# Kernel optimization log

Measured on AMD Instinct MI355X. Metric: run time of the kernel, lower is better.

The kernel has to match this reference:

```python
import jax, jax.numpy as jnp
import numpy as np
from jax.scipy.special import erf

B, S, D = 8, 512, 512
H = 8            # num_heads per half
DH = D // 2      # 256, per-branch model dim
DFF = 2048
HOUT = 2


def _layernorm(x, g, b, eps=1e-6):
    mu = jnp.mean(x, axis=-1, keepdims=True)
    var = jnp.mean(jnp.square(x - mu), axis=-1, keepdims=True)
    return (x - mu) / jnp.sqrt(var + eps) * g + b


def _rescale_dist(w):
    one = jnp.float32(1.0)
    return (one + jnp.exp(one)) / (one + jnp.exp(one - w))


def _mha(xin, wq, bq, wk, bk, wv, bv, wo, bo, maskf, adjoin, dist):
    b, s, dm = xin.shape
    dep = dm // H
    def heads(t):
        return t.reshape(b, s, H, dep).transpose(0, 2, 1, 3)  # (b,h,s,dep)
    q = heads(xin @ wq + bq)
    k = heads(xin @ wk + bk)
    v = heads(xin @ wv + bv)
    scores = jnp.einsum('bhqd,bhkd->bhqk', q, k)
    scale = jnp.sqrt(jnp.float32(dep))
    if dist is not None:
        scores = jax.nn.relu(scores) * _rescale_dist(dist) / scale
    else:
        scores = scores / scale
    scores = scores + maskf * jnp.float32(-1e9)
    if adjoin is not None:
        scores = scores + adjoin
    attn = jax.nn.softmax(scores, axis=-1)
    out = jnp.einsum('bhqk,bhkd->bhqd', attn, v).transpose(0, 2, 1, 3).reshape(b, s, dm)
    return out @ wo + bo, attn


def setup_inputs() -> dict:
    key = jax.random.key(0)
    ks = jax.random.split(key, 32)
    init = lambda k, shp: (jax.random.normal(k, shp, dtype=jnp.float32) * 0.02)
    inp = {
        'x': jax.random.normal(ks[0], (B, S, D), dtype=jnp.float32),
        'adjoin_matrix': jax.random.normal(ks[1], (B, 1, S, S), dtype=jnp.float32),
        'dist_matrix': jax.random.uniform(ks[2], (B, 1, S, S), dtype=jnp.float32),
        # mha1 (adjoin branch)
        'wq1': init(ks[3], (DH, DH)), 'bq1': jnp.zeros((DH,), jnp.float32),
        'wk1': init(ks[4], (DH, DH)), 'bk1': jnp.zeros((DH,), jnp.float32),
        'wv1': init(ks[5], (DH, DH)), 'bv1': jnp.zeros((DH,), jnp.float32),
        'wo1': init(ks[6], (DH, DH)), 'bo1': jnp.zeros((DH,), jnp.float32),
        # mha2 (distance branch)
        'wq2': init(ks[7], (DH, DH)), 'bq2': jnp.zeros((DH,), jnp.float32),
        'wk2': init(ks[8], (DH, DH)), 'bk2': jnp.zeros((DH,), jnp.float32),
        'wv2': init(ks[9], (DH, DH)), 'bv2': jnp.zeros((DH,), jnp.float32),
        'wo2': init(ks[10], (DH, DH)), 'bo2': jnp.zeros((DH,), jnp.float32),
        # BANLayer
        'vnet_w': init(ks[11], (DH, 2 * DH)), 'vnet_b': jnp.zeros((2 * DH,), jnp.float32),
        'qnet_w': init(ks[12], (DH, 2 * DH)), 'qnet_b': jnp.zeros((2 * DH,), jnp.float32),
        'h_mat': init(ks[13], (1, HOUT, 1, 2 * DH)),
        'h_bias': init(ks[14], (1, HOUT, 1, 1)),
        'bn_gamma': jnp.ones((D,), jnp.float32), 'bn_beta': jnp.zeros((D,), jnp.float32),
        'bn_mean': jnp.zeros((D,), jnp.float32), 'bn_var': jnp.ones((D,), jnp.float32),
        # LayerNorms
        'ln1_g': jnp.ones((D,), jnp.float32), 'ln1_b': jnp.zeros((D,), jnp.float32),
        'ln2_g': jnp.ones((D,), jnp.float32), 'ln2_b': jnp.zeros((D,), jnp.float32),
        # FFN
        'ffn_w1': init(ks[15], (D, DFF)), 'ffn_b1': jnp.zeros((DFF,), jnp.float32),
        'ffn_w2': init(ks[16], (DFF, D)), 'ffn_b2': jnp.zeros((D,), jnp.float32),
        # padding mask (int -> cast), 1 = masked
        'encoder_padding_mask': jax.random.randint(ks[17], (B, 1, 1, S), 0, 2, dtype=jnp.int32),
    }
    return inp


def reference(x, adjoin_matrix, dist_matrix,
              wq1, bq1, wk1, bk1, wv1, bv1, wo1, bo1,
              wq2, bq2, wk2, bk2, wv2, bv2, wo2, bo2,
              vnet_w, vnet_b, qnet_w, qnet_b, h_mat, h_bias,
              bn_gamma, bn_beta, bn_mean, bn_var,
              ln1_g, ln1_b, ln2_g, ln2_b,
              ffn_w1, ffn_b1, ffn_w2, ffn_b2,
              encoder_padding_mask):
    maskf = encoder_padding_mask.astype(jnp.float32)
    x1, x2 = jnp.split(x, 2, axis=-1)
    # local branch: adjoin bias, no distance
    x_l, aw_local = _mha(x1, wq1, bq1, wk1, bk1, wv1, bv1, wo1, bo1, maskf, adjoin_matrix, None)
    # global branch: relu + distance rescale, no adjoin
    x_g, aw_global = _mha(x2, wq2, bq2, wk2, bk2, wv2, bv2, wo2, bo2, maskf, None, dist_matrix)
    # BANLayer (h_out=2 <= c, eval mode; p_net is identity for rows=1)
    v_ = jax.nn.relu(x_l @ vnet_w + vnet_b)   # (B,S,2*DH)
    q_ = jax.nn.relu(x_g @ qnet_w + qnet_b)
    att_maps = jnp.einsum('xhyk,bvk,bqk->bhvq', h_mat, v_, q_) + h_bias  # (B,HOUT,S,S)
    logits = jnp.einsum('bvk,bhvq,bqk->bvk', v_, att_maps, q_)           # sum over h
    logits = (logits - bn_mean) / jnp.sqrt(bn_var + 1e-3) * bn_gamma + bn_beta
    attn_output = logits * jnp.concatenate([x_l, x_g], axis=-1)
    out1 = _layernorm(x + attn_output, ln1_g, ln1_b)
    h = out1 @ ffn_w1 + ffn_b1
    h = 0.5 * h * (1.0 + erf(h / jnp.sqrt(jnp.float32(2.0))))  # exact gelu
    ffn_out = h @ ffn_w2 + ffn_b2
    out2 = _layernorm(out1 + ffn_out, ln2_g, ln2_b)
    return (out2, aw_local, aw_global)
```

## Files before the change

### kernel.cpp

```cpp
#include <hip/hip_runtime.h>
#include <hip/hip_bf16.h>

typedef __hip_bfloat16 bf16;
typedef __attribute__((ext_vector_type(8))) short bf16x8;
typedef __attribute__((ext_vector_type(4))) float f32x4;
typedef __attribute__((ext_vector_type(4))) _Float16 f16x4;
typedef unsigned int u32;

#define BB 8
#define SS 512
#define DD 512
#define NH 8
#define DHm 256
#define DFF 2048

__device__ __forceinline__ void gl_lds16(const void* g, void* l) {
  __builtin_amdgcn_global_load_lds((const __attribute__((address_space(1))) void*)g,
                                   (__attribute__((address_space(3))) void*)l, 16, 0, 0);
}

__device__ __forceinline__ bf16x8 cvt8(const float* p) {
  union { bf16x8 v; bf16 h[8]; } u;
  float4 f0 = *(const float4*)p, f1 = *(const float4*)(p + 4);
  u.h[0]=__float2bfloat16(f0.x); u.h[1]=__float2bfloat16(f0.y);
  u.h[2]=__float2bfloat16(f0.z); u.h[3]=__float2bfloat16(f0.w);
  u.h[4]=__float2bfloat16(f1.x); u.h[5]=__float2bfloat16(f1.y);
  u.h[6]=__float2bfloat16(f1.z); u.h[7]=__float2bfloat16(f1.w);
  return u.v;
}

template<int BM, int BN, int SMODE, int BIASM, int ACT, int VTM>
__global__ __launch_bounds__(256)
void gemm2(const bf16* __restrict__ A, const bf16* __restrict__ B,
           const float* __restrict__ bias, float* __restrict__ Cf,
           bf16* __restrict__ Cb, int K, int lda, int ldb, int ldc,
           long long sA, long long sB, long long sC, int sBias,
           bf16* __restrict__ Cb2, const float* __restrict__ cscale)
{
  __shared__ bf16 As[BM * 32];
  __shared__ bf16 Bs[BN * 32];
  const int t = threadIdx.x, lane = t & 63, wave = t >> 6;
  const int l15 = lane & 15, quad = lane >> 4;
  constexpr int WMT = BM / 32, WNT = BN / 32;
  const int wm = (wave & 1) * (BM / 2), wn = (wave >> 1) * (BN / 2);
  const int row0 = blockIdx.y * BM, col0 = blockIdx.x * BN;
  const bf16* Ab = A + (long long)blockIdx.z * sA + (long long)row0 * lda;
  const bf16* Bb = B + (long long)blockIdx.z * sB + (long long)col0 * ldb;
  const int srow = wave * 16 + (lane >> 2), skc = (lane & 3) << 3;

  f32x4 acc[WMT][WNT] = {};

  for (int k0 = 0; k0 < K; k0 += 32) {
#pragma unroll
    for (int j = 0; j < BM / 64; j++)
      gl_lds16(Ab + (long long)(srow + j * 64) * lda + k0 + skc,
               (char*)As + wave * 1024 + j * 4096);
#pragma unroll
    for (int j = 0; j < BN / 64; j++)
      gl_lds16(Bb + (long long)(srow + j * 64) * ldb + k0 + skc,
               (char*)Bs + wave * 1024 + j * 4096);
    __syncthreads();
    bf16x8 af[WMT], bfr[WNT];
#pragma unroll
    for (int i = 0; i < WMT; i++) af[i]  = *(const bf16x8*)&As[(wm + i * 16 + l15) * 32 + quad * 8];
#pragma unroll
    for (int j = 0; j < WNT; j++) bfr[j] = *(const bf16x8*)&Bs[(wn + j * 16 + l15) * 32 + quad * 8];
#pragma unroll
    for (int i = 0; i < WMT; i++)
#pragma unroll
      for (int j = 0; j < WNT; j++)
        acc[i][j] = __builtin_amdgcn_mfma_f32_16x16x32_bf16(af[i], bfr[j], acc[i][j], 0, 0, 0);
    __syncthreads();
  }

  float sb = 0.f;
  if (BIASM == 2) sb = bias[0] + bias[1];
#pragma unroll
  for (int i = 0; i < WMT; i++)
#pragma unroll
    for (int j = 0; j < WNT; j++) {
      int col = col0 + wn + j * 16 + l15;
      float bv = (BIASM == 1) ? bias[(long long)blockIdx.z * sBias + col] : sb;
      float vv[4];
#pragma unroll
      for (int r = 0; r < 4; r++) {
        float v = acc[i][j][r] + bv;
        if (ACT == 1) v = fmaxf(v, 0.f);
        if (ACT == 2) v = 0.5f * v * (1.f + erff(v * 0.70710678118654752f));
        vv[r] = v;
      }
      const int rowb = row0 + wm + i * 16 + (quad << 2);
      if (VTM == 1) {
        const int bidx = rowb >> 9, kpos = rowb & 511;
        const long long zz8 = (long long)blockIdx.z * 8 + bidx;
        if (col < 512) {
          const int part = col >> 8, hh = (col >> 5) & 7, dep = col & 31;
          bf16* dst = Cb2 + (((zz8 * 8 + hh) * 2 + part) * 512 + (long long)kpos) * 32 + dep;
#pragma unroll
          for (int r = 0; r < 4; r++) dst[r * 32] = __float2bfloat16(vv[r]);
        } else {
          const int hh = (col - 512) >> 5, dep = (col - 512) & 31;
          long long vo = ((zz8 * 8 + hh) * 64 + (kpos >> 3)) * 32 + dep;
          bf16 h0 = __float2bfloat16(vv[0]), h1 = __float2bfloat16(vv[1]);
          bf16 h2 = __float2bfloat16(vv[2]), h3 = __float2bfloat16(vv[3]);
          short4 pk;
          pk.x = *(short*)&h0; pk.y = *(short*)&h1; pk.z = *(short*)&h2; pk.w = *(short*)&h3;
          *(short4*)(Cb + vo * 8 + (kpos & 7)) = pk;
        }
      } else {
#pragma unroll
        for (int r = 0; r < 4; r++) {
          long long ci = (long long)blockIdx.z * sC + (long long)(rowb + r) * ldc + col;
          if (SMODE & 1) Cf[ci] = vv[r];
          if (SMODE & 2) Cb[ci] = __float2bfloat16(vv[r]);
          if (VTM == 2) Cb2[ci] = __float2bfloat16(vv[r] * cscale[col]);
        }
      }
    }
}

__global__ __launch_bounds__(256)
void eprep(const float* __restrict__ adjoin, const float* __restrict__ dist,
           const int* __restrict__ mask, _Float16* __restrict__ EP)
{
  const int qt = blockIdx.x, kt = blockIdx.y, zz = blockIdx.z;
  const int b = zz & 7, branch = zz >> 3;
  const float* E = (branch ? dist : adjoin) + ((long long)b * SS + qt * 64) * SS + kt * 128;
  __shared__ float tile[64][129];
  const int t = threadIdx.x;
  const int r0 = t >> 5, c4 = (t & 31) * 4;
#pragma unroll
  for (int jj = 0; jj < 8; jj++) {
    int row = r0 + jj * 8;
    float4 f = *(const float4*)(E + (long long)row * SS + c4);
    tile[row][c4 + 0] = f.x; tile[row][c4 + 1] = f.y;
    tile[row][c4 + 2] = f.z; tile[row][c4 + 3] = f.w;
  }
  __syncthreads();
  const int lane = t & 63, wq = t >> 6, l15 = lane & 15, quad = lane >> 4;
  const float scale_inv = 0.17677669529663688f;
  f16x4* out = (f16x4*)EP;
#pragma unroll
  for (int kcl = 0; kcl < 8; kcl++) {
    int kk = kcl * 16 + l15;
    f16x4 o;
    if (branch == 0) {
      float mv = (float)mask[b * SS + kt * 128 + kk] * -1e9f;
#pragma unroll
      for (int r = 0; r < 4; r++)
        o[r] = (_Float16)(tile[wq * 16 + quad * 4 + r][kk] + mv);
    } else {
#pragma unroll
      for (int r = 0; r < 4; r++) {
        float ev = tile[wq * 16 + quad * 4 + r][kk];
        o[r] = (_Float16)(3.7182818284590452f / (1.f + __expf(1.f - ev)) * scale_inv);
      }
    }
    out[((((long long)zz * 8 + qt) * 4 + wq) * 32 + (kt * 8 + kcl)) * 64 + lane] = o;
  }
}

__global__ __launch_bounds__(256, 2)
void attn_fused(const bf16* __restrict__ QKF, const bf16* __restrict__ VT,
                const int* __restrict__ mask, const _Float16* __restrict__ EP,
                float* __restrict__ awl, float* __restrict__ awg,
                bf16* __restrict__ ctx1, bf16* __restrict__ ctx2)
{
  const int qt = blockIdx.x, h = blockIdx.y, zz = blockIdx.z;
  const int b = zz & 7, branch = zz >> 3;
  float* __restrict__ aw = branch ? awg : awl;
  bf16* __restrict__ ctx = branch ? ctx2 : ctx1;

  const int t = threadIdx.x, lane = t & 63, wave = t >> 6;
  const int l15 = lane & 15, quad = lane >> 4;
  __shared__ bf16x8 Vt[64][32];
  alignas(16) __shared__ bf16 Pl[4][2048];
  __shared__ float mvalf[512];

  const bf16* VTs = VT + ((long long)zz * 8 + h) * 16384;
#pragma unroll
  for (int j = 0; j < 8; j++)
    gl_lds16(VTs + (long long)t * 8 + j * 2048, (char*)Vt + wave * 1024 + j * 4096);

  { int2 m2 = *(const int2*)(mask + b * SS + t * 2);
    mvalf[t * 2]     = (float)m2.x * -1e9f;
    mvalf[t * 2 + 1] = (float)m2.y * -1e9f; }

  const int q0 = qt * 64 + wave * 16;
  const bf16* Qbase = QKF + ((long long)zz * 8 + h) * 2 * 16384;
  const bf16* Kbase = Qbase + 16384;
  bf16x8 qfrag = *(const bf16x8*)(Qbase + (long long)(q0 + l15) * 32 + quad * 8);
  __syncthreads();

  const float scale_inv = 0.17677669529663688f;
  const f16x4* Ep = (const f16x4*)EP + (((long long)zz * 8 + qt) * 4 + wave) * 2048;

  u32 eh[64];
  float rsum[4] = {0.f, 0.f, 0.f, 0.f};
  f32x4 oacc[2] = {};
  short* Pw = (short*)Pl[wave];
  const int rkey = ((l15 >> 2) ^ l15) & 3;

#pragma unroll
  for (int c = 0; c < 4; c++) {
#pragma unroll
    for (int kcl = 0; kcl < 8; kcl++) {
      const int kc = c * 8 + kcl;
      const int kpos = kc * 16 + l15;
      bf16x8 kfrag = *(const bf16x8*)(Kbase + (long long)kpos * 32 + quad * 8);
      f16x4 e4 = Ep[kc * 64 + lane];
      f32x4 a = __builtin_amdgcn_mfma_f32_16x16x32_bf16(qfrag, kfrag, f32x4{0.f,0.f,0.f,0.f}, 0, 0, 0);
      float mv = (branch == 0) ? 0.f : mvalf[kpos];
      u32 p01 = 0, p23 = 0;
#pragma unroll
      for (int r = 0; r < 4; r++) {
        float s = (branch == 0) ? fmaf(a[r], scale_inv, (float)e4[r])
                                : fmaf(fmaxf(a[r], 0.f), (float)e4[r], mv);
        float e = __expf(s);
        rsum[r] += e;
        u32 xb = __float_as_uint(e);
        u32 b16 = (xb + 0x7FFFu + ((xb >> 16) & 1u)) >> 16;
        if (r == 0)      p01 = b16;
        else if (r == 1) p01 |= b16 << 16;
        else if (r == 2) p23 = b16;
        else             p23 |= b16 << 16;
        const int key = (quad ^ r) & 3;
        const int off = (quad * 4 + r) * 256 + (((kcl * 16 + l15) * 2) ^ (key << 5));
        *(short*)((char*)Pw + off) = (short)b16;
      }
      eh[kc * 2]     = p01;
      eh[kc * 2 + 1] = p23;
    }
    __builtin_amdgcn_s_setprio(1);
#pragma unroll
    for (int k2 = 0; k2 < 4; k2++) {
      const int off = l15 * 256 + ((k2 * 64 + quad * 16) ^ (rkey << 5));
      bf16x8 afr = *(const bf16x8*)((const char*)Pw + off);
      const int blk = (c * 4 + k2) * 4 + quad;
      oacc[0] = __builtin_amdgcn_mfma_f32_16x16x32_bf16(afr, Vt[blk][l15],      oacc[0], 0, 0, 0);
      oacc[1] = __builtin_amdgcn_mfma_f32_16x16x32_bf16(afr, Vt[blk][16 + l15], oacc[1], 0, 0, 0);
    }
    __builtin_amdgcn_s_setprio(0);
  }

  float rsi[4];
#pragma unroll
  for (int r = 0; r < 4; r++) {
    float v = rsum[r];
    v += __shfl_xor(v, 1, 16);
    v += __shfl_xor(v, 2, 16);
    v += __shfl_xor(v, 4, 16);
    v += __shfl_xor(v, 8, 16);
    rsi[r] = 1.f / v;
  }

#pragma unroll
  for (int n = 0; n < 2; n++)
#pragma unroll
    for (int r = 0; r < 4; r++) {
      int q = q0 + quad * 4 + r;
      ctx[(long long)(b * SS + q) * DHm + h * 32 + n * 16 + l15] =
          __float2bfloat16(oacc[n][r] * rsi[r]);
    }

  float* awp = aw + (((long long)(b * NH + h) * SS + q0)) * SS;
#pragma unroll
  for (int kc = 0; kc < 32; kc++) {
    u32 p01 = eh[kc * 2], p23 = eh[kc * 2 + 1];
#pragma unroll
    for (int r = 0; r < 4; r++) {
      u32 bits = (r == 0) ? (p01 & 0xFFFFu) : (r == 1) ? (p01 >> 16)
               : (r == 2) ? (p23 & 0xFFFFu) : (p23 >> 16);
      float e = __uint_as_float(bits << 16);
      awp[(long long)(quad * 4 + r) * SS + kc * 16 + l15] = e * rsi[r];
    }
  }
}

__device__ __forceinline__ void tr_tile(const float* __restrict__ src, bf16* __restrict__ dst,
                                        int K, int N, int tile) {
  __shared__ float tl[32][33];
  int tilesN = N >> 5;
  int tk = tile / tilesN, tn = tile % tilesN;
  int c = threadIdx.x & 31, r0 = threadIdx.x >> 5;
#pragma unroll
  for (int i = 0; i < 4; i++) {
    int r = r0 + i * 8;
    tl[r][c] = src[(long long)(tk * 32 + r) * N + tn * 32 + c];
  }
  __syncthreads();
#pragma unroll
  for (int i = 0; i < 4; i++) {
    int r = r0 + i * 8;
    dst[(long long)(tn * 32 + r) * K + tk * 32 + c] = __float2bfloat16(tl[c][r]);
  }
}

__global__ __launch_bounds__(256)
void pack_all(const float* wq1, const float* wk1, const float* wv1,
              const float* wq2, const float* wk2, const float* wv2,
              const float* wo1, const float* wo2,
              const float* vnet_w, const float* qnet_w,
              const float* ffn_w1, const float* ffn_w2,
              const float* bq1, const float* bk1, const float* bv1,
              const float* bq2, const float* bk2, const float* bv2,
              const float* bo1, const float* bo2,
              const float* vnet_b, const float* qnet_b,
              const float* h_mat,
              const float* x,
              bf16* WB1, bf16* WB2, bf16* woT1, bf16* woT2,
              bf16* vnetT, bf16* qnetT, bf16* f1T, bf16* f2T,
              float* BB1v, float* BB2v, float* BOv, float* VQb, float* HSv, bf16* xb)
{
  int blk = blockIdx.x;
  if (blk < 64)        { tr_tile(wq1, WB1,            256, 256, blk); return; }
  if (blk < 128)       { tr_tile(wk1, WB1 + 256*256,  256, 256, blk-64); return; }
  if (blk < 192)       { tr_tile(wv1, WB1 + 512*256,  256, 256, blk-128); return; }
  if (blk < 256)       { tr_tile(wq2, WB2,            256, 256, blk-192); return; }
  if (blk < 320)       { tr_tile(wk2, WB2 + 256*256,  256, 256, blk-256); return; }
  if (blk < 384)       { tr_tile(wv2, WB2 + 512*256,  256, 256, blk-320); return; }
  if (blk < 448)       { tr_tile(wo1, woT1,           256, 256, blk-384); return; }
  if (blk < 512)       { tr_tile(wo2, woT2,           256, 256, blk-448); return; }
  if (blk < 640)       { tr_tile(vnet_w, vnetT,       256, 512, blk-512); return; }
  if (blk < 768)       { tr_tile(qnet_w, qnetT,       256, 512, blk-640); return; }
  if (blk < 1792)      { tr_tile(ffn_w1, f1T,         512, 2048, blk-768); return; }
  if (blk < 2816)      { tr_tile(ffn_w2, f2T,         2048, 512, blk-1792); return; }
  if (blk < 3840) {
    long long i0 = (long long)(blk - 2816) * 2048 + threadIdx.x * 8;
    *(bf16x8*)(xb + i0) = cvt8(x + i0);
    return;
  }
  if (blk < 3846) {
    int b = blk - 3840;
    const float* src = b==0?bq1 : b==1?bk1 : b==2?bv1 : b==3?bq2 : b==4?bk2 : bv2;
    float* dst = (b < 3 ? BB1v : BB2v) + (b % 3) * 256;
    dst[threadIdx.x] = src[threadIdx.x];
    return;
  }
  if (blk < 3848) {
    int b = blk - 3846;
    BOv[b * 256 + threadIdx.x] = (b ? bo2 : bo1)[threadIdx.x];
    return;
  }
  if (blk < 3852) {
    int b = blk - 3848;
    const float* src = (b < 2) ? vnet_b : qnet_b;
    VQb[b * 256 + threadIdx.x] = src[(b & 1) * 256 + threadIdx.x];
    return;
  }
  {
    int t = threadIdx.x;
    HSv[t]       = h_mat[t]       + h_mat[512 + t];
    HSv[t + 256] = h_mat[256 + t] + h_mat[768 + t];
  }
}

__global__ __launch_bounds__(256)
void tr_qn(const bf16* __restrict__ Qn, bf16* __restrict__ QnT)
{
  int b = blockIdx.z, tk = blockIdx.y, tn = blockIdx.x;
  __shared__ bf16 tl[32][33];
  int c = threadIdx.x & 31, r0 = threadIdx.x >> 5;
  const bf16* src = Qn + (long long)b * 512 * 512;
  bf16* dst = QnT + (long long)b * 512 * 512;
#pragma unroll
  for (int i = 0; i < 4; i++) { int r = r0 + i * 8; tl[r][c] = src[(tk * 32 + r) * 512 + tn * 32 + c]; }
  __syncthreads();
#pragma unroll
  for (int i = 0; i < 4; i++) { int r = r0 + i * 8; dst[(tn * 32 + r) * 512 + tk * 32 + c] = tl[c][r]; }
}

__global__ __launch_bounds__(256)
void bn_gate_ln1_kernel(const float* __restrict__ x, const bf16* __restrict__ vbuf,
                        const float* __restrict__ T, const float* __restrict__ xl,
                        const float* __restrict__ xg,
                        const float* __restrict__ bng, const float* __restrict__ bnb,
                        const float* __restrict__ bnm, const float* __restrict__ bnv,
                        const float* __restrict__ lng, const float* __restrict__ lnb,
                        float* __restrict__ out1, bf16* __restrict__ out1b)
{
  const int row = blockIdx.x;
  const int t = threadIdx.x;
  const int lane = t & 63, wave = t >> 6;
  __shared__ float red[8];
  float val[2];
#pragma unroll
  for (int i = 0; i < 2; i++) {
    int c = t + i * 256;
    long long idx = (long long)row * DD + c;
    float lg = __bfloat162float(vbuf[idx]) * T[idx];
    float bn = (lg - bnm[c]) / sqrtf(bnv[c] + 1e-3f) * bng[c] + bnb[c];
    float gate = (c < DHm) ? xl[(long long)row * DHm + c] : xg[(long long)row * DHm + (c - DHm)];
    val[i] = x[idx] + bn * gate;
  }
  float s = val[0] + val[1];
#pragma unroll
  for (int o = 32; o > 0; o >>= 1) s += __shfl_xor(s, o);
  if (lane == 0) red[wave] = s;
  __syncthreads();
  float mu = (red[0] + red[1] + red[2] + red[3]) * (1.f / 512.f);
  float d0 = val[0] - mu, d1 = val[1] - mu;
  float vs = d0 * d0 + d1 * d1;
#pragma unroll
  for (int o = 32; o > 0; o >>= 1) vs += __shfl_xor(vs, o);
  if (lane == 0) red[4 + wave] = vs;
  __syncthreads();
  float inv = 1.f / sqrtf((red[4] + red[5] + red[6] + red[7]) * (1.f / 512.f) + 1e-6f);
  float o0 = d0 * inv * lng[t] + lnb[t];
  float o1 = d1 * inv * lng[t + 256] + lnb[t + 256];
  out1[(long long)row * DD + t] = o0;
  out1[(long long)row * DD + t + 256] = o1;
  out1b[(long long)row * DD + t] = __float2bfloat16(o0);
  out1b[(long long)row * DD + t + 256] = __float2bfloat16(o1);
}

__global__ __launch_bounds__(256)
void ln2_kernel(const float* __restrict__ a, const float* __restrict__ b2,
                const float* __restrict__ g, const float* __restrict__ bta,
                float* __restrict__ out)
{
  const int row = blockIdx.x;
  const int t = threadIdx.x;
  const int lane = t & 63, wave = t >> 6;
  __shared__ float red[8];
  float v0 = a[(long long)row * DD + t]       + b2[(long long)row * DD + t];
  float v1 = a[(long long)row * DD + t + 256] + b2[(long long)row * DD + t + 256];
  float s = v0 + v1;
#pragma unroll
  for (int o = 32; o > 0; o >>= 1) s += __shfl_xor(s, o);
  if (lane == 0) red[wave] = s;
  __syncthreads();
  float mu = (red[0] + red[1] + red[2] + red[3]) * (1.f / 512.f);
  float d0 = v0 - mu, d1 = v1 - mu;
  float vs = d0 * d0 + d1 * d1;
#pragma unroll
  for (int o = 32; o > 0; o >>= 1) vs += __shfl_xor(vs, o);
  if (lane == 0) red[4 + wave] = vs;
  __syncthreads();
  float inv = 1.f / sqrtf((red[4] + red[5] + red[6] + red[7]) * (1.f / 512.f) + 1e-6f);
  out[(long long)row * DD + t]       = d0 * inv * g[t]       + bta[t];
  out[(long long)row * DD + t + 256] = d1 * inv * g[t + 256] + bta[t + 256];
}

extern "C" void kernel_launch(void* const* d_in, const int* in_sizes, int n_in,
                              void* d_out, int out_size, void* d_ws, size_t ws_size,
                              hipStream_t stream) {
  const float* x      = (const float*)d_in[0];
  const float* adjoin = (const float*)d_in[1];
  const float* dist   = (const float*)d_in[2];
  const float* wq1=(const float*)d_in[3],  *bq1=(const float*)d_in[4];
  const float* wk1=(const float*)d_in[5],  *bk1=(const float*)d_in[6];
  const float* wv1=(const float*)d_in[7],  *bv1=(const float*)d_in[8];
  const float* wo1=(const float*)d_in[9],  *bo1=(const float*)d_in[10];
  const float* wq2=(const float*)d_in[11], *bq2=(const float*)d_in[12];
  const float* wk2=(const float*)d_in[13], *bk2=(const float*)d_in[14];
  const float* wv2=(const float*)d_in[15], *bv2=(const float*)d_in[16];
  const float* wo2=(const float*)d_in[17], *bo2=(const float*)d_in[18];
  const float* vnet_w=(const float*)d_in[19], *vnet_b=(const float*)d_in[20];
  const float* qnet_w=(const float*)d_in[21], *qnet_b=(const float*)d_in[22];
  const float* h_mat=(const float*)d_in[23], *h_bias=(const float*)d_in[24];
  const float* bn_g=(const float*)d_in[25], *bn_b=(const float*)d_in[26];
  const float* bn_m=(const float*)d_in[27], *bn_v=(const float*)d_in[28];
  const float* ln1_g=(const float*)d_in[29], *ln1_b=(const float*)d_in[30];
  const float* ln2_g=(const float*)d_in[31], *ln2_b=(const float*)d_in[32];
  const float* ffn_w1=(const float*)d_in[33], *ffn_b1=(const float*)d_in[34];
  const float* ffn_w2=(const float*)d_in[35], *ffn_b2=(const float*)d_in[36];
  const int* mask = (const int*)d_in[37];

  char* base = (char*)d_ws;
  size_t off = 0;
  auto alloc = [&](size_t bytes) { char* p = base + off; off += (bytes + 255) & ~(size_t)255; return p; };
  bf16*  xb    = (bf16*) alloc(4096LL*512*2);
  bf16*  WB1   = (bf16*) alloc(768*256*2);
  bf16*  WB2   = (bf16*) alloc(768*256*2);
  float* BB1v  = (float*)alloc(768*4);
  float* BB2v  = (float*)alloc(768*4);
  float* BOv   = (float*)alloc(512*4);
  float* VQb   = (float*)alloc(1024*4);
  float* HSv   = (float*)alloc(512*4);
  bf16*  woT1  = (bf16*) alloc(256*256*2);
  bf16*  woT2  = (bf16*) alloc(256*256*2);
  bf16*  vnetT = (bf16*) alloc(512*256*2);
  bf16*  qnetT = (bf16*) alloc(512*256*2);
  bf16*  f1T   = (bf16*) alloc(2048*512*2);
  bf16*  f2T   = (bf16*) alloc(512*2048*2);
  bf16*  QKF   = (bf16*) alloc(16LL*8*2*512*32*2);
  bf16*  VTb   = (bf16*) alloc(2LL*8*8*512*32*2);
  _Float16* EP = (_Float16*)alloc(8388608);
  bf16*  CTX   = (bf16*) alloc(4096LL*256*2);
  bf16*  CTX2  = (bf16*) alloc(4096LL*256*2);
  float* XL    = (float*)alloc(4096LL*256*4);
  float* XG    = (float*)alloc(4096LL*256*4);
  bf16*  XLb   = (bf16*) alloc(4096LL*256*2);
  bf16*  XGb   = (bf16*) alloc(4096LL*256*2);
  bf16*  Vn    = (bf16*) alloc(4096LL*512*2);
  bf16*  Qn    = (bf16*) alloc(4096LL*512*2);
  bf16*  QnT   = (bf16*) alloc(4096LL*512*2);
  bf16*  VH    = (bf16*) alloc(4096LL*512*2);
  bf16*  G     = (bf16*) alloc(8LL*512*512*2);
  float* T     = (float*)alloc(4096LL*512*4);
  float* OUT1  = (float*)alloc(4096LL*512*4);
  bf16*  OUT1b = (bf16*) alloc(4096LL*512*2);
  bf16*  H     = (bf16*) alloc(4096LL*2048*2);
  float* FFNO  = (float*)alloc(4096LL*512*4);

  float* out2 = (float*)d_out;
  float* awl  = out2 + 2097152LL;
  float* awg  = awl + 16777216LL;

  const int MR = BB * SS;
  const long long GST = (long long)SS * SS;

  pack_all<<<dim3(3853), 256, 0, stream>>>(
      wq1, wk1, wv1, wq2, wk2, wv2, wo1, wo2, vnet_w, qnet_w, ffn_w1, ffn_w2,
      bq1, bk1, bv1, bq2, bk2, bv2, bo1, bo2, vnet_b, qnet_b, h_mat, x,
      WB1, WB2, woT1, woT2, vnetT, qnetT, f1T, f2T, BB1v, BB2v, BOv, VQb, HSv, xb);

  eprep<<<dim3(8, 4, 16), 256, 0, stream>>>(adjoin, dist, mask, EP);

  gemm2<128,128,0,1,0,1><<<dim3(6, 32, 2), 256, 0, stream>>>(
      xb, WB1, BB1v, nullptr, VTb, 256, 512, 256, 768,
      256LL, 768LL*256, 0LL, 768, QKF, nullptr);

  attn_fused<<<dim3(8, NH, 16), 256, 0, stream>>>(
      QKF, VTb, mask, EP, awl, awg, CTX, CTX2);

  gemm2<64,128,3,1,0,0><<<dim3(2, 64, 2), 256, 0, stream>>>(
      CTX, woT1, BOv, XL, XLb, 256, 256, 256, 256,
      4096LL*256, 256LL*256, 4096LL*256, 256, nullptr, nullptr);

  gemm2<128,128,2,1,1,2><<<dim3(4, 32, 2), 256, 0, stream>>>(
      XLb, vnetT, VQb, nullptr, Vn, 256, 256, 256, 512,
      4096LL*256, 512LL*256, 4096LL*512, 512, VH, HSv);

  tr_qn<<<dim3(16, 16, BB), 256, 0, stream>>>(Qn, QnT);
  gemm2<64,128,2,2,0,0><<<dim3(4, 8, BB), 256, 0, stream>>>(
      VH, Qn, h_bias, nullptr, G, 512, 512, 512, 512, GST, GST, GST, 0, nullptr, nullptr);
  gemm2<64,128,1,0,0,0><<<dim3(4, 8, BB), 256, 0, stream>>>(
      G, QnT, nullptr, T, nullptr, 512, 512, 512, 512, GST, GST, GST, 0, nullptr, nullptr);

  bn_gate_ln1_kernel<<<dim3(MR), 256, 0, stream>>>(
      x, Vn, T, XL, XG, bn_g, bn_b, bn_m, bn_v, ln1_g, ln1_b, OUT1, OUT1b);

  gemm2<128,128,2,1,2,0><<<dim3(16, 32, 1), 256, 0, stream>>>(
      OUT1b, f1T, ffn_b1, nullptr, H, 512, 512, 512, 2048, 0, 0, 0, 0, nullptr, nullptr);
  gemm2<64,128,1,1,0,0><<<dim3(4, 64, 1), 256, 0, stream>>>(
      H, f2T, ffn_b2, FFNO, nullptr, 2048, 2048, 2048, 512, 0, 0, 0, 0, nullptr, nullptr);

  ln2_kernel<<<dim3(MR), 256, 0, stream>>>(OUT1, FFNO, ln2_g, ln2_b, out2);
}
```

Before: 463.9 us.

## Double-buffer GEMM LDS tiles, fold eprep into pack kernel, shrink GEMM tiles

The GEMM main loop now double-buffers its A/B tiles in LDS, so the global-to-LDS copy of the next K slice is issued before the MFMAs on the current slice, with one barrier per iteration. The separate eprep launch is merged into pack_all as extra blocks, which saves one kernel launch. Several GEMMs move from 64x128 or 128x128 tiles to 64x64 tiles to give more blocks and better CU occupancy on the smaller problems. The costs are twice the LDS per block and lower data reuse per tile with the smaller tiles.

```diff
diff --git a/kernel.cpp b/kernel.cpp
--- a/kernel.cpp
+++ b/kernel.cpp
@@ -29,6 +29,18 @@
   return u.v;
 }
 
+#define STAGE_G(buf, k0)                                                   \
+  {                                                                        \
+    _Pragma("unroll")                                                      \
+    for (int j = 0; j < BM / 64; j++)                                      \
+      gl_lds16(Ab + (long long)(srow + j * 64) * lda + (k0) + skc,         \
+               (char*)As[buf] + wave * 1024 + j * 4096);                   \
+    _Pragma("unroll")                                                      \
+    for (int j = 0; j < BN / 64; j++)                                      \
+      gl_lds16(Bb + (long long)(srow + j * 64) * ldb + (k0) + skc,         \
+               (char*)Bs[buf] + wave * 1024 + j * 4096);                   \
+  }
+
 template<int BM, int BN, int SMODE, int BIASM, int ACT, int VTM>
 __global__ __launch_bounds__(256)
 void gemm2(const bf16* __restrict__ A, const bf16* __restrict__ B,
@@ -37,8 +49,8 @@
            long long sA, long long sB, long long sC, int sBias,
            bf16* __restrict__ Cb2, const float* __restrict__ cscale)
 {
-  __shared__ bf16 As[BM * 32];
-  __shared__ bf16 Bs[BN * 32];
+  __shared__ bf16 As[2][BM * 32];
+  __shared__ bf16 Bs[2][BN * 32];
   const int t = threadIdx.x, lane = t & 63, wave = t >> 6;
   const int l15 = lane & 15, quad = lane >> 4;
   constexpr int WMT = BM / 32, WNT = BN / 32;
@@ -50,27 +62,26 @@
 
   f32x4 acc[WMT][WNT] = {};
 
+  STAGE_G(0, 0)
+  asm volatile("s_waitcnt vmcnt(0)" ::: "memory");
+  __builtin_amdgcn_s_barrier();
+
+  int cur = 0;
   for (int k0 = 0; k0 < K; k0 += 32) {
-#pragma unroll
-    for (int j = 0; j < BM / 64; j++)
-      gl_lds16(Ab + (long long)(srow + j * 64) * lda + k0 + skc,
-               (char*)As + wave * 1024 + j * 4096);
-#pragma unroll
-    for (int j = 0; j < BN / 64; j++)
-      gl_lds16(Bb + (long long)(srow + j * 64) * ldb + k0 + skc,
-               (char*)Bs + wave * 1024 + j * 4096);
-    __syncthreads();
+    if (k0 + 32 < K) STAGE_G(cur ^ 1, k0 + 32)
     bf16x8 af[WMT], bfr[WNT];
 #pragma unroll
-    for (int i = 0; i < WMT; i++) af[i]  = *(const bf16x8*)&As[(wm + i * 16 + l15) * 32 + quad * 8];
-#pragma unroll
-    for (int j = 0; j < WNT; j++) bfr[j] = *(const bf16x8*)&Bs[(wn + j * 16 + l15) * 32 + quad * 8];
+    for (int i = 0; i < WMT; i++) af[i]  = *(const bf16x8*)&As[cur][(wm + i * 16 + l15) * 32 + quad * 8];
+#pragma unroll
+    for (int j = 0; j < WNT; j++) bfr[j] = *(const bf16x8*)&Bs[cur][(wn + j * 16 + l15) * 32 + quad * 8];
 #pragma unroll
     for (int i = 0; i < WMT; i++)
 #pragma unroll
       for (int j = 0; j < WNT; j++)
         acc[i][j] = __builtin_amdgcn_mfma_f32_16x16x32_bf16(af[i], bfr[j], acc[i][j], 0, 0, 0);
-    __syncthreads();
+    asm volatile("s_waitcnt vmcnt(0)" ::: "memory");
+    __builtin_amdgcn_s_barrier();
+    cur ^= 1;
   }
 
   float sb = 0.f;
@@ -117,47 +128,6 @@
         }
       }
     }
-}
-
-__global__ __launch_bounds__(256)
-void eprep(const float* __restrict__ adjoin, const float* __restrict__ dist,
-           const int* __restrict__ mask, _Float16* __restrict__ EP)
-{
-  const int qt = blockIdx.x, kt = blockIdx.y, zz = blockIdx.z;
-  const int b = zz & 7, branch = zz >> 3;
-  const float* E = (branch ? dist : adjoin) + ((long long)b * SS + qt * 64) * SS + kt * 128;
-  __shared__ float tile[64][129];
-  const int t = threadIdx.x;
-  const int r0 = t >> 5, c4 = (t & 31) * 4;
-#pragma unroll
-  for (int jj = 0; jj < 8; jj++) {
-    int row = r0 + jj * 8;
-    float4 f = *(const float4*)(E + (long long)row * SS + c4);
-    tile[row][c4 + 0] = f.x; tile[row][c4 + 1] = f.y;
-    tile[row][c4 + 2] = f.z; tile[row][c4 + 3] = f.w;
-  }
-  __syncthreads();
-  const int lane = t & 63, wq = t >> 6, l15 = lane & 15, quad = lane >> 4;
-  const float scale_inv = 0.17677669529663688f;
-  f16x4* out = (f16x4*)EP;
-#pragma unroll
-  for (int kcl = 0; kcl < 8; kcl++) {
-    int kk = kcl * 16 + l15;
-    f16x4 o;
-    if (branch == 0) {
-      float mv = (float)mask[b * SS + kt * 128 + kk] * -1e9f;
-#pragma unroll
-      for (int r = 0; r < 4; r++)
-        o[r] = (_Float16)(tile[wq * 16 + quad * 4 + r][kk] + mv);
-    } else {
-#pragma unroll
-      for (int r = 0; r < 4; r++) {
-        float ev = tile[wq * 16 + quad * 4 + r][kk];
-        o[r] = (_Float16)(3.7182818284590452f / (1.f + __expf(1.f - ev)) * scale_inv);
-      }
-    }
-    out[((((long long)zz * 8 + qt) * 4 + wq) * 32 + (kt * 8 + kcl)) * 64 + lane] = o;
-  }
 }
 
 __global__ __launch_bounds__(256, 2)
@@ -308,9 +278,11 @@
               const float* vnet_b, const float* qnet_b,
               const float* h_mat,
               const float* x,
+              const float* adjoin, const float* dist, const int* mask,
               bf16* WB1, bf16* WB2, bf16* woT1, bf16* woT2,
               bf16* vnetT, bf16* qnetT, bf16* f1T, bf16* f2T,
-              float* BB1v, float* BB2v, float* BOv, float* VQb, float* HSv, bf16* xb)
+              float* BB1v, float* BB2v, float* BOv, float* VQb, float* HSv,
+              bf16* xb, _Float16* EP)
 {
   int blk = blockIdx.x;
   if (blk < 64)        { tr_tile(wq1, WB1,            256, 256, blk); return; }
@@ -348,10 +320,49 @@
     VQb[b * 256 + threadIdx.x] = src[(b & 1) * 256 + threadIdx.x];
     return;
   }
-  {
+  if (blk < 3853) {
     int t = threadIdx.x;
     HSv[t]       = h_mat[t]       + h_mat[512 + t];
     HSv[t + 256] = h_mat[256 + t] + h_mat[768 + t];
+    return;
+  }
+  {
+    const int e = blk - 3853;
+    const int qt = e & 7, kt = (e >> 3) & 3, zz = e >> 5;
+    const int b = zz & 7, branch = zz >> 3;
+    const float* E = (branch ? dist : adjoin) + ((long long)b * SS + qt * 64) * SS + kt * 128;
+    __shared__ float tile[64][129];
+    const int t = threadIdx.x;
+    const int r0 = t >> 5, c4 = (t & 31) * 4;
+#pragma unroll
+    for (int jj = 0; jj < 8; jj++) {
+      int row = r0 + jj * 8;
+      float4 f = *(const float4*)(E + (long long)row * SS + c4);
+      tile[row][c4 + 0] = f.x; tile[row][c4 + 1] = f.y;
+      tile[row][c4 + 2] = f.z; tile[row][c4 + 3] = f.w;
+    }
+    __syncthreads();
+    const int lane = t & 63, wq = t >> 6, l15 = lane & 15, quad = lane >> 4;
+    const float scale_inv = 0.17677669529663688f;
+    f16x4* out = (f16x4*)EP;
+#pragma unroll
+    for (int kcl = 0; kcl < 8; kcl++) {
+      int kk = kcl * 16 + l15;
+      f16x4 o;
+      if (branch == 0) {
+        float mv = (float)mask[b * SS + kt * 128 + kk] * -1e9f;
+#pragma unroll
+        for (int r = 0; r < 4; r++)
+          o[r] = (_Float16)(tile[wq * 16 + quad * 4 + r][kk] + mv);
+      } else {
+#pragma unroll
+        for (int r = 0; r < 4; r++) {
+          float ev = tile[wq * 16 + quad * 4 + r][kk];
+          o[r] = (_Float16)(3.7182818284590452f / (1.f + __expf(1.f - ev)) * scale_inv);
+        }
+      }
+      out[((((long long)zz * 8 + qt) * 4 + wq) * 32 + (kt * 8 + kcl)) * 64 + lane] = o;
+    }
   }
 }
 
@@ -511,12 +522,12 @@
   const int MR = BB * SS;
   const long long GST = (long long)SS * SS;
 
-  pack_all<<<dim3(3853), 256, 0, stream>>>(
+  pack_all<<<dim3(4365), 256, 0, stream>>>(
       wq1, wk1, wv1, wq2, wk2, wv2, wo1, wo2, vnet_w, qnet_w, ffn_w1, ffn_w2,
       bq1, bk1, bv1, bq2, bk2, bv2, bo1, bo2, vnet_b, qnet_b, h_mat, x,
-      WB1, WB2, woT1, woT2, vnetT, qnetT, f1T, f2T, BB1v, BB2v, BOv, VQb, HSv, xb);
-
-  eprep<<<dim3(8, 4, 16), 256, 0, stream>>>(adjoin, dist, mask, EP);
+      adjoin, dist, mask,
+      WB1, WB2, woT1, woT2, vnetT, qnetT, f1T, f2T, BB1v, BB2v, BOv, VQb, HSv,
+      xb, EP);
 
   gemm2<128,128,0,1,0,1><<<dim3(6, 32, 2), 256, 0, stream>>>(
       xb, WB1, BB1v, nullptr, VTb, 256, 512, 256, 768,
@@ -525,18 +536,18 @@
   attn_fused<<<dim3(8, NH, 16), 256, 0, stream>>>(
       QKF, VTb, mask, EP, awl, awg, CTX, CTX2);
 
-  gemm2<64,128,3,1,0,0><<<dim3(2, 64, 2), 256, 0, stream>>>(
+  gemm2<64,64,3,1,0,0><<<dim3(4, 64, 2), 256, 0, stream>>>(
       CTX, woT1, BOv, XL, XLb, 256, 256, 256, 256,
       4096LL*256, 256LL*256, 4096LL*256, 256, nullptr, nullptr);
 
-  gemm2<128,128,2,1,1,2><<<dim3(4, 32, 2), 256, 0, stream>>>(
+  gemm2<64,64,2,1,1,2><<<dim3(8, 64, 2), 256, 0, stream>>>(
       XLb, vnetT, VQb, nullptr, Vn, 256, 256, 256, 512,
       4096LL*256, 512LL*256, 4096LL*512, 512, VH, HSv);
 
   tr_qn<<<dim3(16, 16, BB), 256, 0, stream>>>(Qn, QnT);
-  gemm2<64,128,2,2,0,0><<<dim3(4, 8, BB), 256, 0, stream>>>(
+  gemm2<64,64,2,2,0,0><<<dim3(8, 8, BB), 256, 0, stream>>>(
       VH, Qn, h_bias, nullptr, G, 512, 512, 512, 512, GST, GST, GST, 0, nullptr, nullptr);
-  gemm2<64,128,1,0,0,0><<<dim3(4, 8, BB), 256, 0, stream>>>(
+  gemm2<64,64,1,0,0,0><<<dim3(8, 8, BB), 256, 0, stream>>>(
       G, QnT, nullptr, T, nullptr, 512, 512, 512, 512, GST, GST, GST, 0, nullptr, nullptr);
 
   bn_gate_ln1_kernel<<<dim3(MR), 256, 0, stream>>>(
@@ -544,7 +555,7 @@
 
   gemm2<128,128,2,1,2,0><<<dim3(16, 32, 1), 256, 0, stream>>>(
       OUT1b, f1T, ffn_b1, nullptr, H, 512, 512, 512, 2048, 0, 0, 0, 0, nullptr, nullptr);
-  gemm2<64,128,1,1,0,0><<<dim3(4, 64, 1), 256, 0, stream>>>(
+  gemm2<64,64,1,1,0,0><<<dim3(8, 64, 1), 256, 0, stream>>>(
       H, f2T, ffn_b2, FFNO, nullptr, 2048, 2048, 2048, 512, 0, 0, 0, 0, nullptr, nullptr);
 
   ln2_kernel<<<dim3(MR), 256, 0, stream>>>(OUT1, FFNO, ln2_g, ln2_b, out2);
```

New measurement: 444.4 us. -4.2%, faster.
